# Optimization experiments

Measured on AMD Instinct MI355X. Metric: run time of the kernel, lower is better.

## Reference

```python
import jax, jax.numpy as jnp
import numpy as np
import math

B, F, M, H, W, PD, KS = 2048, 512, 16, 32, 32, 64, 11
K = KS * KS
R = KS // 2
SIGMA = float(KS) / 3.0
HW = H * W


def _pos_encoding(gaze):
    # (B,2) -> (B,PD); interleaved sin/cos per axis
    half = PD // 2
    div = jnp.exp(jnp.arange(0, half, 2, dtype=jnp.float32) * -(math.log(10000.0) / half))  # (half/2,)
    def enc(p):  # p: (B,1)
        s = jnp.sin(p * div)
        c = jnp.cos(p * div)
        return jnp.stack([s, c], axis=-1).reshape(-1, half)
    return jnp.concatenate([enc(gaze[:, 0:1]), enc(gaze[:, 1:2])], axis=1)


def _adaptive_avg_pool3(x):
    # x: (B,C,H,W) -> (B,C,3,3), matching torch AdaptiveAvgPool2d(3)
    def bounds(n):
        return [(int(np.floor(i * n / 3)), int(np.ceil((i + 1) * n / 3))) for i in range(3)]
    hb, wb = bounds(x.shape[2]), bounds(x.shape[3])
    rows = []
    for (h0, h1) in hb:
        cols = [x[:, :, h0:h1, w0:w1].mean(axis=(2, 3)) for (w0, w1) in wb]
        rows.append(jnp.stack(cols, axis=-1))
    return jnp.stack(rows, axis=-2)  # (B,C,3,3)


def _conv(x, k, b):
    y = jax.lax.conv_general_dilated(x, k, (1, 1), 'SAME',
                                     dimension_numbers=('NCHW', 'OIHW', 'NCHW'))
    return y + b[None, :, None, None]


def setup_inputs() -> dict:
    key = jax.random.key(0)
    ks = jax.random.split(key, 20)
    n = lambda i, shp, sc=0.02: (jax.random.normal(ks[i], shp, dtype=jnp.float32) * sc)
    inp = {
        'features': jax.random.normal(ks[0], (B, F), dtype=jnp.float32),
        'cell_state': jax.random.normal(ks[1], (B, M, H, W), dtype=jnp.float32),
        'gaze_coords': jax.random.uniform(ks[2], (B, 2), dtype=jnp.float32),
        # input_gate: Linear(F+PD,256) -> ReLU -> Linear(256,128) -> ReLU
        'w1': n(3, (F + PD, 256)), 'b1': jnp.zeros((256,), jnp.float32),
        'w2': n(4, (256, 128)), 'b2': jnp.zeros((128,), jnp.float32),
        # write_value: Linear(128, M*K)
        'wv': n(5, (128, M * K)), 'bv': jnp.zeros((M * K,), jnp.float32),
        # strength_head: Linear(2M,64) -> ReLU -> Linear(64,1) -> Sigmoid
        'ws1': n(6, (2 * M, 64)), 'bs1': jnp.zeros((64,), jnp.float32),
        'ws2': n(7, (64, 1)), 'bs2': jnp.zeros((1,), jnp.float32),
        # output_gate convs + final linear
        'ck1': n(8, (128, M, 3, 3)), 'cb1': jnp.zeros((128,), jnp.float32),
        'ck2': n(9, (64, 128, 3, 3)), 'cb2': jnp.zeros((64,), jnp.float32),
        'wo': n(10, (64 * 9, 64 * 9)), 'bo': jnp.zeros((64 * 9,), jnp.float32),
    }
    return inp


def reference(features, cell_state, gaze_coords, w1, b1, w2, b2, wv, bv,
              ws1, bs1, ws2, bs2, ck1, cb1, ck2, cb2, wo, bo):
    # --- input gate + write values ---
    pe = _pos_encoding(gaze_coords)
    g = jax.nn.relu(jnp.concatenate([features, pe], axis=1) @ w1 + b1)
    g = jax.nn.relu(g @ w2 + b2)
    write_vals = (g @ wv + bv).reshape(B, K, M)

    # --- neighborhood geometry ---
    offs = jnp.arange(-R, R + 1)
    ox, oy = jnp.meshgrid(offs, offs, indexing='xy')
    ox, oy = ox.reshape(-1), oy.reshape(-1)  # (K,)
    gx = jnp.clip(gaze_coords[:, 0] * (W - 1), 0.0, W - 1.0)
    gy = jnp.clip(gaze_coords[:, 1] * (H - 1), 0.0, H - 1.0)
    x0 = jnp.floor(gx).astype(jnp.int32)
    y0 = jnp.floor(gy).astype(jnp.int32)
    xs = jnp.clip(x0[:, None] + ox[None, :], 0, W - 1)  # (B,K)
    ys = jnp.clip(y0[:, None] + oy[None, :], 0, H - 1)
    dx = xs.astype(jnp.float32) - gx[:, None]
    dy = ys.astype(jnp.float32) - gy[:, None]
    gauss = jnp.exp(-(dx * dx + dy * dy) / max(1e-6, 2.0 * SIGMA ** 2))
    nw = gauss / jnp.maximum(gauss.sum(axis=1, keepdims=True), 1e-8)  # (B,K)

    # --- gather previous values ---
    idx = ys * W + xs  # (B,K) flat indices
    cell_flat = cell_state.reshape(B, M, HW)
    prev = jnp.take_along_axis(cell_flat, idx[:, None, :], axis=2).transpose(0, 2, 1)  # (B,K,M)

    # --- learned per-cell strength gate ---
    gate_in = jnp.concatenate([prev, write_vals], axis=-1)  # (B,K,2M)
    s = jax.nn.relu(gate_in @ ws1 + bs1)
    gstr = jax.nn.sigmoid(s @ ws2 + bs2)  # (B,K,1)
    w_all = nw[:, :, None] * gstr  # (B,K,1)
    new_vals = (1.0 - w_all) * prev + w_all * write_vals  # (B,K,M)

    # --- weighted scatter-add with normalization ---
    b_idx = jnp.arange(B)[:, None]
    den = jnp.zeros((B, HW), jnp.float32).at[b_idx, idx].add(w_all[..., 0])
    num = jnp.zeros((B, HW, M), jnp.float32).at[b_idx, idx].add(w_all * new_vals)
    keep = 1.0 - jnp.minimum(den, 1.0)  # (B,HW)
    updated_flat = keep[:, None, :] * cell_flat + num.transpose(0, 2, 1)
    updated = updated_flat.reshape(B, M, H, W)

    # --- output gate ---
    y = jax.nn.relu(_conv(updated, ck1, cb1))
    y = jax.nn.relu(_conv(y, ck2, cb2))
    y = _adaptive_avg_pool3(y).reshape(B, -1)  # (B,576)
    out = y @ wo + bo
    return out, updated
```

## Files before the change

### kernel.cpp

```cpp
#include <hip/hip_runtime.h>
#include <hip/hip_bf16.h>
#include <math.h>

#define NB 2048
#define NF 512
#define NM 16
#define NK 121
#define NMK 1936

typedef __attribute__((ext_vector_type(8))) short bf16x8;
typedef __attribute__((ext_vector_type(4))) float f32x4;

#define MFMA __builtin_amdgcn_mfma_f32_16x16x32_bf16

static __device__ __forceinline__ unsigned short f2b(float f) {
  unsigned int u = __float_as_uint(f);
  unsigned int lsb = (u >> 16) & 1u;
  u += 0x7fffu + lsb;
  return (unsigned short)(u >> 16);
}

static __device__ __forceinline__ unsigned cvtpk(float lo, float hi) {
  unsigned r;
  asm("v_cvt_pk_bf16_f32 %0, %1, %2" : "=v"(r) : "v"(lo), "v"(hi));
  return r;
}

__global__ __launch_bounds__(256) void k_pack(
    const float* __restrict__ ck1, const float* __restrict__ ck2,
    unsigned short* __restrict__ ap1, unsigned short* __restrict__ ap2) {
  int i = blockIdx.x * 256 + threadIdx.x;
  if (i < 20480) {
    int j = i & 7, lane = (i >> 3) & 63;
    int m2 = (i >> 9) & 1, kc = (i >> 10) % 5, w = i / 5120;
    int c1 = w * 32 + m2 * 16 + (lane & 15);
    int k = kc * 32 + ((lane >> 4) << 3) + j;
    int s = k >> 4, ci = k & 15;
    float v = 0.f;
    if (s < 9) v = ck1[((c1 * 16 + ci) * 3 + s / 3) * 3 + (s % 3)];
    ap1[i] = f2b(v);
  }
  int i2 = i - 20480;
  if (i2 >= 0 && i2 < 73728) {
    int j = i2 & 7, lane = (i2 >> 3) & 63;
    int kc = (i2 >> 9) & 3, s = (i2 >> 11) % 9, mt = i2 / 18432;
    int c2 = mt * 16 + (lane & 15);
    int c1 = kc * 32 + ((lane >> 4) << 3) + j;
    float v = ck2[((c2 * 128 + c1) * 3 + s / 3) * 3 + (s % 3)];
    ap2[i2] = f2b(v);
  }
}

__global__ __launch_bounds__(256) void k_mlp(
    const float* __restrict__ feat, const float* __restrict__ gaze,
    const float* __restrict__ w1, const float* __restrict__ b1,
    const float* __restrict__ w2, const float* __restrict__ b2,
    const float* __restrict__ wv, const float* __restrict__ bv,
    float* __restrict__ wvout) {
  __shared__ float xs[8][576];
  __shared__ float g1[8][256];
  __shared__ float g2[8][128];
  const int t = threadIdx.x;
  const int b0 = blockIdx.x * 8;

  for (int e = t; e < 8 * 512; e += 256) {
    int r = e >> 9, i = e & 511;
    xs[r][i] = feat[(size_t)(b0 + r) * NF + i];
  }
  for (int e = t; e < 8 * 64; e += 256) {
    int r = e >> 6, i = e & 63;
    int axis = i >> 5;
    int ii = i & 31;
    int jj = ii >> 1;
    int isc = ii & 1;
    float p = gaze[(size_t)(b0 + r) * 2 + axis];
    float dv = expf(-(float)(2 * jj) * 0.28782313662425575f);
    float ang = p * dv;
    xs[r][512 + i] = isc ? cosf(ang) : sinf(ang);
  }
  __syncthreads();
  {
    float acc[8];
    float bb = b1[t];
#pragma unroll
    for (int r = 0; r < 8; r++) acc[r] = bb;
    for (int i = 0; i < 576; i++) {
      float w = w1[(size_t)i * 256 + t];
#pragma unroll
      for (int r = 0; r < 8; r++) acc[r] = fmaf(xs[r][i], w, acc[r]);
    }
#pragma unroll
    for (int r = 0; r < 8; r++) g1[r][t] = fmaxf(acc[r], 0.f);
  }
  __syncthreads();
  if (t < 128) {
    float acc[8];
    float bb = b2[t];
#pragma unroll
    for (int r = 0; r < 8; r++) acc[r] = bb;
    for (int i = 0; i < 256; i++) {
      float w = w2[(size_t)i * 128 + t];
#pragma unroll
      for (int r = 0; r < 8; r++) acc[r] = fmaf(g1[r][i], w, acc[r]);
    }
#pragma unroll
    for (int r = 0; r < 8; r++) g2[r][t] = fmaxf(acc[r], 0.f);
  }
  __syncthreads();
  for (int j = t; j < NMK; j += 256) {
    float acc[8];
    float bb = bv[j];
#pragma unroll
    for (int r = 0; r < 8; r++) acc[r] = bb;
    for (int i = 0; i < 128; i++) {
      float w = wv[(size_t)i * NMK + j];
#pragma unroll
      for (int r = 0; r < 8; r++) acc[r] = fmaf(g2[r][i], w, acc[r]);
    }
#pragma unroll
    for (int r = 0; r < 8; r++) wvout[(size_t)(b0 + r) * NMK + j] = acc[r];
  }
}

__global__ __launch_bounds__(256) void k_update(
    const float* __restrict__ cell, const float* __restrict__ gaze,
    const float* __restrict__ wvin,
    const float* __restrict__ ws1, const float* __restrict__ bs1,
    const float* __restrict__ ws2, const float* __restrict__ bs2,
    float* __restrict__ updated, unsigned short* __restrict__ ubf) {
  __shared__ float numl[16][129];
  __shared__ float denl[128];
  __shared__ float ws1s[2048];
  __shared__ float bs1s[64];
  __shared__ float ws2s[64];
  __shared__ float nws[121];
  __shared__ float gsum_s;
  __shared__ float bs2s;
  const int t = threadIdx.x;
  const int b = blockIdx.x;

  for (int e = t; e < 16 * 129; e += 256) ((float*)numl)[e] = 0.f;
  if (t < 128) denl[t] = 0.f;
  for (int e = t; e < 2048; e += 256) ws1s[e] = ws1[e];
  if (t < 64) { bs1s[t] = bs1[t]; ws2s[t] = ws2[t]; }
  if (t == 0) bs2s = bs2[0];

  const float gx = fminf(fmaxf(gaze[(size_t)b * 2 + 0] * 31.f, 0.f), 31.f);
  const float gy = fminf(fmaxf(gaze[(size_t)b * 2 + 1] * 31.f, 0.f), 31.f);
  const int x0 = (int)floorf(gx);
  const int y0 = (int)floorf(gy);
  const int wx0 = max(0, x0 - 5);
  const int wy0 = max(0, y0 - 5);

  int xi = 0, yi = 0;
  if (t < NK) {
    int ox = t % 11 - 5;
    int oy = t / 11 - 5;
    xi = min(max(x0 + ox, 0), 31);
    yi = min(max(y0 + oy, 0), 31);
    float dx = (float)xi - gx, dy = (float)yi - gy;
    nws[t] = expf(-(dx * dx + dy * dy) * (9.0f / 242.0f));
  }
  __syncthreads();
  if (t == 0) {
    float s = 0.f;
    for (int k = 0; k < NK; k++) s += nws[k];
    gsum_s = fmaxf(s, 1e-8f);
  }
  __syncthreads();

  if (t < NK) {
    const float nw = nws[t] / gsum_s;
    const int idx = yi * 32 + xi;
    const int local = (yi - wy0) * 11 + (xi - wx0);
    float prev[16], wvv[16];
#pragma unroll
    for (int m = 0; m < 16; m++) prev[m] = cell[(size_t)b * 16384 + m * 1024 + idx];
#pragma unroll
    for (int m = 0; m < 16; m++) wvv[m] = wvin[(size_t)b * NMK + t * 16 + m];
    float z2 = bs2s;
    for (int j = 0; j < 64; j++) {
      float z = bs1s[j];
#pragma unroll
      for (int i = 0; i < 16; i++) z = fmaf(prev[i], ws1s[i * 64 + j], z);
#pragma unroll
      for (int i = 0; i < 16; i++) z = fmaf(wvv[i], ws1s[(16 + i) * 64 + j], z);
      z = fmaxf(z, 0.f);
      z2 = fmaf(z, ws2s[j], z2);
    }
    float gstr = 1.f / (1.f + expf(-z2));
    float w = nw * gstr;
    atomicAdd(&denl[local], w);
#pragma unroll
    for (int m = 0; m < 16; m++) {
      float nv = (1.f - w) * prev[m] + w * wvv[m];
      atomicAdd(&numl[m][local], w * nv);
    }
  }
  __syncthreads();

  for (int e = t; e < 16384; e += 256) {
    int m = e >> 10, hw = e & 1023;
    int yy = hw >> 5, xx = hw & 31;
    int wy = yy - wy0, wx = xx - wx0;
    float dv = 0.f, nm = 0.f;
    if ((unsigned)wy < 11u && (unsigned)wx < 11u) {
      int local = wy * 11 + wx;
      dv = denl[local];
      nm = numl[m][local];
    }
    float keep = 1.f - fminf(dv, 1.f);
    updated[(size_t)b * 16384 + e] = keep * cell[(size_t)b * 16384 + e] + nm;
  }

  unsigned* ub32 = (unsigned*)ubf + (size_t)b * 9248;
  for (int e = t; e < 8192; e += 256) {
    int p = e & 7;
    int hw = e >> 3;
    int yy = hw >> 5, xx = hw & 31;
    int wy = yy - wy0, wx = xx - wx0;
    float dv = 0.f, n0 = 0.f, n1 = 0.f;
    if ((unsigned)wy < 11u && (unsigned)wx < 11u) {
      int local = wy * 11 + wx;
      dv = denl[local];
      n0 = numl[2 * p][local];
      n1 = numl[2 * p + 1][local];
    }
    float keep = 1.f - fminf(dv, 1.f);
    float v0 = keep * cell[(size_t)b * 16384 + (2 * p) * 1024 + hw] + n0;
    float v1 = keep * cell[(size_t)b * 16384 + (2 * p + 1) * 1024 + hw] + n1;
    ub32[((yy + 1) * 34 + (xx + 1)) * 8 + p] = cvtpk(v0, v1);
  }
  for (int e = t; e < 1056; e += 256) {
    int j = e & 7, pos = e >> 3;
    int row, col;
    if (pos < 34)       { row = 0;             col = pos; }
    else if (pos < 68)  { row = 33;            col = pos - 34; }
    else if (pos < 100) { row = pos - 68 + 1;  col = 0; }
    else                { row = pos - 100 + 1; col = 33; }
    ub32[(row * 34 + col) * 8 + j] = 0u;
  }
}

__global__ __launch_bounds__(256, 2) void k_conv3(
    const unsigned short* __restrict__ ubf,
    const unsigned short* __restrict__ ap1, const float* __restrict__ cb1,
    const unsigned short* __restrict__ ap2, const float* __restrict__ cb2,
    float* __restrict__ ypool) {
  __shared__ unsigned short y1[6][34][136];
  const int t = threadIdx.x;
  const int b = blockIdx.x;
  const int lane = t & 63;
  const int w = t >> 6;
  const int ln = lane & 15;
  const int q = lane >> 4;
  const int qh = q >> 1, ql = q & 1;

  const unsigned short* ubb = ubf + (size_t)b * 18496;

  bf16x8 a2[9][4];
#pragma unroll
  for (int s = 0; s < 9; s++)
#pragma unroll
    for (int kc = 0; kc < 4; kc++)
      a2[s][kc] = *(const bf16x8*)(ap2 + (size_t)((w * 36 + s * 4 + kc) * 64 + lane) * 8);

  f32x4 cb2r;
  {
    int c2b = w * 16 + q * 4;
    cb2r = f32x4{cb2[c2b], cb2[c2b + 1], cb2[c2b + 2], cb2[c2b + 3]};
  }

  int po1[5];
#pragma unroll
  for (int kc = 0; kc < 5; kc++) {
    int s = 2 * kc + qh;
    if (s > 8) s = 0;
    po1[kc] = (s / 3) * 544 + (s % 3) * 16;
  }

  for (int e = t; e < 816; e += 256) {
    int w8 = e % 68;
    int r2 = e / 68;
    ((unsigned*)y1)[(r2 >> 1) * 2312 + ((r2 & 1) ? 2244 : 0) + w8] = 0u;
  }

  f32x4 PL0 = {0.f, 0.f, 0.f, 0.f}, PL1 = PL0, PL2 = PL0;
  f32x4 PH0 = PL0, PH1 = PL0, PH2 = PL0;

#pragma unroll 1
  for (int ti = 0; ti < 8; ti++) {
    const int r0 = ti * 4;

    bf16x8 a1[5][2];
#pragma unroll
    for (int kc = 0; kc < 5; kc++)
#pragma unroll
      for (int m2 = 0; m2 < 2; m2++)
        a1[kc][m2] = *(const bf16x8*)(ap1 + (size_t)(((w * 5 + kc) * 2 + m2) * 64 + lane) * 8);
    f32x4 cb1r[2];
#pragma unroll
    for (int m2 = 0; m2 < 2; m2++) {
      int c1b = w * 32 + m2 * 16 + q * 4;
      cb1r[m2] = f32x4{cb1[c1b], cb1[c1b + 1], cb1[c1b + 2], cb1[c1b + 3]};
    }

#pragma unroll 2
    for (int nt = 0; nt < 12; nt++) {
      const int ry = nt >> 1, h = nt & 1;
      const int gy1 = r0 - 1 + ry;
      const int gyc = min(max(gy1, 0), 31);
      const int x = h * 16 + ln;
      const unsigned short* bp = ubb + gyc * 544 + x * 16 + ql * 8;
      bf16x8 f0 = *(const bf16x8*)(bp + po1[0]);
      bf16x8 f1 = *(const bf16x8*)(bp + po1[1]);
      bf16x8 f2 = *(const bf16x8*)(bp + po1[2]);
      bf16x8 f3 = *(const bf16x8*)(bp + po1[3]);
      bf16x8 f4 = *(const bf16x8*)(bp + po1[4]);
      f32x4 acc0 = cb1r[0], acc1 = cb1r[1];
      acc0 = MFMA(a1[0][0], f0, acc0, 0, 0, 0); acc1 = MFMA(a1[0][1], f0, acc1, 0, 0, 0);
      acc0 = MFMA(a1[1][0], f1, acc0, 0, 0, 0); acc1 = MFMA(a1[1][1], f1, acc1, 0, 0, 0);
      acc0 = MFMA(a1[2][0], f2, acc0, 0, 0, 0); acc1 = MFMA(a1[2][1], f2, acc1, 0, 0, 0);
      acc0 = MFMA(a1[3][0], f3, acc0, 0, 0, 0); acc1 = MFMA(a1[3][1], f3, acc1, 0, 0, 0);
      acc0 = MFMA(a1[4][0], f4, acc0, 0, 0, 0); acc1 = MFMA(a1[4][1], f4, acc1, 0, 0, 0);
      const bool inr = ((unsigned)gy1 < 32u);
#pragma unroll
      for (int m2 = 0; m2 < 2; m2++) {
        f32x4 a = m2 ? acc1 : acc0;
        float v0 = inr ? fmaxf(a[0], 0.f) : 0.f;
        float v1 = inr ? fmaxf(a[1], 0.f) : 0.f;
        float v2 = inr ? fmaxf(a[2], 0.f) : 0.f;
        float v3 = inr ? fmaxf(a[3], 0.f) : 0.f;
        uint2 pk;
        pk.x = cvtpk(v0, v1);
        pk.y = cvtpk(v2, v3);
        *(uint2*)&y1[ry][1 + x][w * 32 + m2 * 16 + q * 4] = pk;
      }
    }
    __syncthreads();

#pragma unroll
    for (int h = 0; h < 2; h++) {
      const int xg = h * 16 + ln;
      const unsigned short* yb = &y1[0][xg][q * 8];
      f32x4 A0 = cb2r, A1 = cb2r, A2 = cb2r, A3 = cb2r;
#pragma unroll
      for (int yr = 0; yr < 6; yr++)
#pragma unroll
        for (int kc = 0; kc < 4; kc++)
#pragma unroll
          for (int dx = 0; dx < 3; dx++) {
            bf16x8 fr = *(const bf16x8*)(yb + yr * 4624 + dx * 136 + kc * 32);
#pragma unroll
            for (int dy = 0; dy < 3; dy++) {
              const int rr = yr - dy;
              if (rr < 0 || rr > 3) continue;
              f32x4& ac = (rr == 0) ? A0 : ((rr == 1) ? A1 : ((rr == 2) ? A2 : A3));
              ac = MFMA(a2[dy * 3 + dx][kc], fr, ac, 0, 0, 0);
            }
          }
#pragma unroll
      for (int rr = 0; rr < 4; rr++) {
        const int grow = r0 + rr;
        const float rm0 = (grow <= 10) ? 1.f : 0.f;
        const float rm1 = (grow >= 10 && grow <= 21) ? 1.f : 0.f;
        const float rm2 = (grow >= 21) ? 1.f : 0.f;
        f32x4 v = (rr == 0) ? A0 : ((rr == 1) ? A1 : ((rr == 2) ? A2 : A3));
        v[0] = fmaxf(v[0], 0.f);
        v[1] = fmaxf(v[1], 0.f);
        v[2] = fmaxf(v[2], 0.f);
        v[3] = fmaxf(v[3], 0.f);
        if (h == 0) {
          PL0 += v * rm0; PL1 += v * rm1; PL2 += v * rm2;
        } else {
          PH0 += v * rm0; PH1 += v * rm1; PH2 += v * rm2;
        }
      }
    }
    __syncthreads();
  }

  const float mA0 = (ln <= 10) ? 1.f : 0.f;
  const float mA1 = (ln >= 10) ? 1.f : 0.f;
  const float mB1 = (ln <= 5) ? 1.f : 0.f;
  const float mB2 = (ln >= 5) ? 1.f : 0.f;
  f32x4 t00 = PL0 * mA0, t01 = PL0 * mA1 + PH0 * mB1, t02 = PH0 * mB2;
  f32x4 t10 = PL1 * mA0, t11 = PL1 * mA1 + PH1 * mB1, t12 = PH1 * mB2;
  f32x4 t20 = PL2 * mA0, t21 = PL2 * mA1 + PH2 * mB1, t22 = PH2 * mB2;

  {
    f32x4* tv[9] = {&t00, &t01, &t02, &t10, &t11, &t12, &t20, &t21, &t22};
#pragma unroll
    for (int i = 0; i < 9; i++) {
      f32x4& v = *tv[i];
#pragma unroll
      for (int c = 0; c < 4; c++) {
        float s = v[c];
        s += __shfl_xor(s, 1, 64);
        s += __shfl_xor(s, 2, 64);
        s += __shfl_xor(s, 4, 64);
        s += __shfl_xor(s, 8, 64);
        v[c] = s;
      }
    }
  }

  float* yp = ypool + (size_t)b * 576 + (w * 16 + q * 4) * 9;
#define PWRITE(tv, ph, pw)                                                      \
  if (ln == (ph * 3 + pw)) {                                                    \
    const float dv = 1.f / (float)(((ph == 1) ? 12 : 11) * ((pw == 1) ? 12 : 11)); \
    yp[0 * 9 + ph * 3 + pw] = tv[0] * dv;                                       \
    yp[1 * 9 + ph * 3 + pw] = tv[1] * dv;                                       \
    yp[2 * 9 + ph * 3 + pw] = tv[2] * dv;                                       \
    yp[3 * 9 + ph * 3 + pw] = tv[3] * dv;                                       \
  }
  PWRITE(t00, 0, 0) PWRITE(t01, 0, 1) PWRITE(t02, 0, 2)
  PWRITE(t10, 1, 0) PWRITE(t11, 1, 1) PWRITE(t12, 1, 2)
  PWRITE(t20, 2, 0) PWRITE(t21, 2, 1) PWRITE(t22, 2, 2)
#undef PWRITE
}

__global__ __launch_bounds__(256) void k_out(
    const float* __restrict__ ypool, const float* __restrict__ wo,
    const float* __restrict__ bo, float* __restrict__ out) {
  __shared__ float ys[8][576];
  const int t = threadIdx.x;
  const int b0 = blockIdx.x * 8;
  for (int e = t; e < 8 * 576; e += 256) {
    int r = e / 576, i = e % 576;
    ys[r][i] = ypool[(size_t)(b0 + r) * 576 + i];
  }
  __syncthreads();
  for (int j = t; j < 576; j += 256) {
    float acc[8];
    float bb = bo[j];
#pragma unroll
    for (int r = 0; r < 8; r++) acc[r] = bb;
    for (int i = 0; i < 576; i++) {
      float w = wo[(size_t)i * 576 + j];
#pragma unroll
      for (int r = 0; r < 8; r++) acc[r] = fmaf(ys[r][i], w, acc[r]);
    }
#pragma unroll
    for (int r = 0; r < 8; r++) out[(size_t)(b0 + r) * 576 + j] = acc[r];
  }
}

extern "C" void kernel_launch(void* const* d_in, const int* in_sizes, int n_in,
                              void* d_out, int out_size, void* d_ws, size_t ws_size,
                              hipStream_t stream) {
  (void)in_sizes; (void)n_in; (void)out_size;
  const float* feat = (const float*)d_in[0];
  const float* cell = (const float*)d_in[1];
  const float* gaze = (const float*)d_in[2];
  const float* w1   = (const float*)d_in[3];
  const float* b1   = (const float*)d_in[4];
  const float* w2   = (const float*)d_in[5];
  const float* b2   = (const float*)d_in[6];
  const float* wv   = (const float*)d_in[7];
  const float* bv   = (const float*)d_in[8];
  const float* ws1  = (const float*)d_in[9];
  const float* bs1  = (const float*)d_in[10];
  const float* ws2  = (const float*)d_in[11];
  const float* bs2  = (const float*)d_in[12];
  const float* ck1  = (const float*)d_in[13];
  const float* cb1  = (const float*)d_in[14];
  const float* ck2  = (const float*)d_in[15];
  const float* cb2  = (const float*)d_in[16];
  const float* wo   = (const float*)d_in[17];
  const float* bo   = (const float*)d_in[18];

  float* out0    = (float*)d_out;
  float* updated = out0 + (size_t)NB * 576;
  float* wvout   = (float*)d_ws;
  float* ypool   = wvout + (size_t)NB * NMK;
  unsigned short* ap1 = (unsigned short*)(ypool + (size_t)NB * 576);
  unsigned short* ap2 = ap1 + 20480;
  unsigned short* ubf = ap2 + 73728;

  const size_t fixed_bytes = ((size_t)NB * (NMK + 576)) * 4 + (size_t)94208 * 2;
  const size_t wsz = ws_size ? ws_size : ((size_t)1 << 30);
  int chunk = 512;
  while (chunk > 128 && fixed_bytes + (size_t)chunk * 36992 > wsz) chunk >>= 1;

  k_pack<<<dim3(368), dim3(256), 0, stream>>>(ck1, ck2, ap1, ap2);
  k_mlp<<<dim3(NB / 8), dim3(256), 0, stream>>>(feat, gaze, w1, b1, w2, b2, wv, bv, wvout);
  for (int b0 = 0; b0 < NB; b0 += chunk) {
    const int n = (NB - b0 < chunk) ? (NB - b0) : chunk;
    k_update<<<dim3(n), dim3(256), 0, stream>>>(
        cell + (size_t)b0 * 16384, gaze + (size_t)b0 * 2,
        wvout + (size_t)b0 * NMK, ws1, bs1, ws2, bs2,
        updated + (size_t)b0 * 16384, ubf);
    k_conv3<<<dim3(n), dim3(256), 0, stream>>>(
        ubf, ap1, cb1, ap2, cb2, ypool + (size_t)b0 * 576);
  }
  k_out<<<dim3(NB / 8), dim3(256), 0, stream>>>(ypool, wo, bo, out0);
}
```

Measured before the change: 1.279 ms.

## Rebalance MLP and update kernels across threads and enlarge batch chunk

k_mlp now handles 4 rows per block instead of 8, doubling the grid, and its write_value projection gives each thread 7+1 column accumulators held in registers. k_update splits the strength-gate MLP across both halves of the block, uses all 256 threads instead of 121, and replaces the serial normalizer sum with a wave shuffle reduction. Unroll pragmas are added to the inner loops, and the default update/conv chunk grows to the full batch so fewer launches are needed. The aim is better occupancy and parallelism in the small kernels. The cost is that each weight matrix is re-read by twice as many blocks and the workspace needs are larger.

```diff
diff --git a/kernel.cpp b/kernel.cpp
--- a/kernel.cpp
+++ b/kernel.cpp
@@ -57,18 +57,18 @@
     const float* __restrict__ w2, const float* __restrict__ b2,
     const float* __restrict__ wv, const float* __restrict__ bv,
     float* __restrict__ wvout) {
-  __shared__ float xs[8][576];
-  __shared__ float g1[8][256];
-  __shared__ float g2[8][128];
+  __shared__ float xs[4][576];
+  __shared__ float g1[4][256];
+  __shared__ float g2[4][128];
   const int t = threadIdx.x;
-  const int b0 = blockIdx.x * 8;
-
-  for (int e = t; e < 8 * 512; e += 256) {
+  const int b0 = blockIdx.x * 4;
+
+  for (int e = t; e < 4 * 512; e += 256) {
     int r = e >> 9, i = e & 511;
     xs[r][i] = feat[(size_t)(b0 + r) * NF + i];
   }
-  for (int e = t; e < 8 * 64; e += 256) {
-    int r = e >> 6, i = e & 63;
+  if (t < 4 * 64) {
+    int r = t >> 6, i = t & 63;
     int axis = i >> 5;
     int ii = i & 31;
     int jj = ii >> 1;
@@ -80,45 +80,74 @@
   }
   __syncthreads();
   {
-    float acc[8];
+    float acc[4];
     float bb = b1[t];
 #pragma unroll
-    for (int r = 0; r < 8; r++) acc[r] = bb;
+    for (int r = 0; r < 4; r++) acc[r] = bb;
+#pragma unroll 8
     for (int i = 0; i < 576; i++) {
       float w = w1[(size_t)i * 256 + t];
 #pragma unroll
-      for (int r = 0; r < 8; r++) acc[r] = fmaf(xs[r][i], w, acc[r]);
-    }
-#pragma unroll
-    for (int r = 0; r < 8; r++) g1[r][t] = fmaxf(acc[r], 0.f);
+      for (int r = 0; r < 4; r++) acc[r] = fmaf(xs[r][i], w, acc[r]);
+    }
+#pragma unroll
+    for (int r = 0; r < 4; r++) g1[r][t] = fmaxf(acc[r], 0.f);
   }
   __syncthreads();
   if (t < 128) {
-    float acc[8];
+    float acc[4];
     float bb = b2[t];
 #pragma unroll
-    for (int r = 0; r < 8; r++) acc[r] = bb;
+    for (int r = 0; r < 4; r++) acc[r] = bb;
+#pragma unroll 8
     for (int i = 0; i < 256; i++) {
       float w = w2[(size_t)i * 128 + t];
 #pragma unroll
-      for (int r = 0; r < 8; r++) acc[r] = fmaf(g1[r][i], w, acc[r]);
-    }
-#pragma unroll
-    for (int r = 0; r < 8; r++) g2[r][t] = fmaxf(acc[r], 0.f);
-  }
-  __syncthreads();
-  for (int j = t; j < NMK; j += 256) {
-    float acc[8];
-    float bb = bv[j];
-#pragma unroll
-    for (int r = 0; r < 8; r++) acc[r] = bb;
+      for (int r = 0; r < 4; r++) acc[r] = fmaf(g1[r][i], w, acc[r]);
+    }
+#pragma unroll
+    for (int r = 0; r < 4; r++) g2[r][t] = fmaxf(acc[r], 0.f);
+  }
+  __syncthreads();
+  {
+    float acc7[7][4];
+    float accT[4];
+#pragma unroll
+    for (int jj = 0; jj < 7; jj++) {
+      float bb = bv[t + 256 * jj];
+#pragma unroll
+      for (int r = 0; r < 4; r++) acc7[jj][r] = bb;
+    }
+    {
+      float bb = (t < 144) ? bv[1792 + t] : 0.f;
+#pragma unroll
+      for (int r = 0; r < 4; r++) accT[r] = bb;
+    }
+#pragma unroll 2
     for (int i = 0; i < 128; i++) {
-      float w = wv[(size_t)i * NMK + j];
-#pragma unroll
-      for (int r = 0; r < 8; r++) acc[r] = fmaf(g2[r][i], w, acc[r]);
-    }
-#pragma unroll
-    for (int r = 0; r < 8; r++) wvout[(size_t)(b0 + r) * NMK + j] = acc[r];
+      float g[4];
+#pragma unroll
+      for (int r = 0; r < 4; r++) g[r] = g2[r][i];
+      const float* wrow = wv + (size_t)i * NMK;
+#pragma unroll
+      for (int jj = 0; jj < 7; jj++) {
+        float w = wrow[t + 256 * jj];
+#pragma unroll
+        for (int r = 0; r < 4; r++) acc7[jj][r] = fmaf(g[r], w, acc7[jj][r]);
+      }
+      if (t < 144) {
+        float w = wrow[1792 + t];
+#pragma unroll
+        for (int r = 0; r < 4; r++) accT[r] = fmaf(g[r], w, accT[r]);
+      }
+    }
+#pragma unroll
+    for (int r = 0; r < 4; r++) {
+      float* orow = wvout + (size_t)(b0 + r) * NMK;
+#pragma unroll
+      for (int jj = 0; jj < 7; jj++) orow[t + 256 * jj] = acc7[jj][r];
+      if (t < 144) orow[1792 + t] = accT[r];
+    }
   }
 }
 
@@ -134,10 +163,13 @@
   __shared__ float bs1s[64];
   __shared__ float ws2s[64];
   __shared__ float nws[121];
+  __shared__ float z2part[2][128];
   __shared__ float gsum_s;
   __shared__ float bs2s;
   const int t = threadIdx.x;
   const int b = blockIdx.x;
+  const int kk = t & 127;
+  const int hf = t >> 7;
 
   for (int e = t; e < 16 * 129; e += 256) ((float*)numl)[e] = 0.f;
   if (t < 128) denl[t] = 0.f;
@@ -153,41 +185,55 @@
   const int wy0 = max(0, y0 - 5);
 
   int xi = 0, yi = 0;
-  if (t < NK) {
-    int ox = t % 11 - 5;
-    int oy = t / 11 - 5;
+  if (kk < NK) {
+    int ox = kk % 11 - 5;
+    int oy = kk / 11 - 5;
     xi = min(max(x0 + ox, 0), 31);
     yi = min(max(y0 + oy, 0), 31);
-    float dx = (float)xi - gx, dy = (float)yi - gy;
-    nws[t] = expf(-(dx * dx + dy * dy) * (9.0f / 242.0f));
-  }
-  __syncthreads();
-  if (t == 0) {
-    float s = 0.f;
-    for (int k = 0; k < NK; k++) s += nws[k];
-    gsum_s = fmaxf(s, 1e-8f);
+    if (hf == 0) {
+      float dx = (float)xi - gx, dy = (float)yi - gy;
+      nws[kk] = expf(-(dx * dx + dy * dy) * (9.0f / 242.0f));
+    }
+  }
+  __syncthreads();
+  if (t < 64) {
+    float s = nws[t] + ((t + 64 < NK) ? nws[t + 64] : 0.f);
+    s += __shfl_xor(s, 1, 64);
+    s += __shfl_xor(s, 2, 64);
+    s += __shfl_xor(s, 4, 64);
+    s += __shfl_xor(s, 8, 64);
+    s += __shfl_xor(s, 16, 64);
+    s += __shfl_xor(s, 32, 64);
+    if (t == 0) gsum_s = fmaxf(s, 1e-8f);
+  }
+  __syncthreads();
+
+  float prev[16], wvv[16];
+  if (kk < NK) {
+    const int idx = yi * 32 + xi;
+#pragma unroll
+    for (int m = 0; m < 16; m++) prev[m] = cell[(size_t)b * 16384 + m * 1024 + idx];
+#pragma unroll
+    for (int m = 0; m < 16; m++) wvv[m] = wvin[(size_t)b * NMK + kk * 16 + m];
+    float z2p = 0.f;
+    const int j0 = hf * 32;
+    for (int j = j0; j < j0 + 32; j++) {
+      float z = bs1s[j];
+#pragma unroll
+      for (int i = 0; i < 16; i++) z = fmaf(prev[i], ws1s[i * 64 + j], z);
+#pragma unroll
+      for (int i = 0; i < 16; i++) z = fmaf(wvv[i], ws1s[(16 + i) * 64 + j], z);
+      z = fmaxf(z, 0.f);
+      z2p = fmaf(z, ws2s[j], z2p);
+    }
+    z2part[hf][kk] = z2p;
   }
   __syncthreads();
 
   if (t < NK) {
     const float nw = nws[t] / gsum_s;
-    const int idx = yi * 32 + xi;
     const int local = (yi - wy0) * 11 + (xi - wx0);
-    float prev[16], wvv[16];
-#pragma unroll
-    for (int m = 0; m < 16; m++) prev[m] = cell[(size_t)b * 16384 + m * 1024 + idx];
-#pragma unroll
-    for (int m = 0; m < 16; m++) wvv[m] = wvin[(size_t)b * NMK + t * 16 + m];
-    float z2 = bs2s;
-    for (int j = 0; j < 64; j++) {
-      float z = bs1s[j];
-#pragma unroll
-      for (int i = 0; i < 16; i++) z = fmaf(prev[i], ws1s[i * 64 + j], z);
-#pragma unroll
-      for (int i = 0; i < 16; i++) z = fmaf(wvv[i], ws1s[(16 + i) * 64 + j], z);
-      z = fmaxf(z, 0.f);
-      z2 = fmaf(z, ws2s[j], z2);
-    }
+    float z2 = bs2s + z2part[0][t] + z2part[1][t];
     float gstr = 1.f / (1.f + expf(-z2));
     float w = nw * gstr;
     atomicAdd(&denl[local], w);
@@ -436,6 +482,7 @@
     float bb = bo[j];
 #pragma unroll
     for (int r = 0; r < 8; r++) acc[r] = bb;
+#pragma unroll 4
     for (int i = 0; i < 576; i++) {
       float w = wo[(size_t)i * 576 + j];
 #pragma unroll
@@ -480,11 +527,11 @@
 
   const size_t fixed_bytes = ((size_t)NB * (NMK + 576)) * 4 + (size_t)94208 * 2;
   const size_t wsz = ws_size ? ws_size : ((size_t)1 << 30);
-  int chunk = 512;
+  int chunk = 2048;
   while (chunk > 128 && fixed_bytes + (size_t)chunk * 36992 > wsz) chunk >>= 1;
 
   k_pack<<<dim3(368), dim3(256), 0, stream>>>(ck1, ck2, ap1, ap2);
-  k_mlp<<<dim3(NB / 8), dim3(256), 0, stream>>>(feat, gaze, w1, b1, w2, b2, wv, bv, wvout);
+  k_mlp<<<dim3(NB / 4), dim3(256), 0, stream>>>(feat, gaze, w1, b1, w2, b2, wv, bv, wvout);
   for (int b0 = 0; b0 < NB; b0 += chunk) {
     const int n = (NB - b0 < chunk) ? (NB - b0) : chunk;
     k_update<<<dim3(n), dim3(256), 0, stream>>>(
```

Measured after the change: 1.093 ms. 14.5% less time.
